# Kernel optimization log

Hardware: AMD Instinct MI355X
Metric: run time of the kernel (lower is better)

## Reference

```python
import jax, jax.numpy as jnp
import numpy as np

B, S, DIM = 2, 2048, 1024
N_HEAD, HEAD_DIM = 16, 64


def setup_inputs() -> dict:
    key = jax.random.key(0)
    k1, k2, k3, k4 = jax.random.split(key, 4)
    x = jax.random.normal(k1, (B, S, DIM), dtype=jnp.float32)
    # rotary table: cos/sin pairs, shape [S, head_dim//2, 2]
    half = HEAD_DIM // 2
    inv_freq = 1.0 / (10000.0 ** (jnp.arange(0, half, dtype=jnp.float32) / half))
    t = jnp.arange(S, dtype=jnp.float32)
    ang = t[:, None] * inv_freq[None, :]
    freqs_cis = jnp.stack([jnp.cos(ang), jnp.sin(ang)], axis=-1)  # [S, half, 2]
    # causal boolean mask [1,1,S,S] (True = attend)
    mask = jnp.tril(jnp.ones((S, S), dtype=bool))[None, None]
    wqkv = jax.random.normal(k2, (3 * DIM, DIM), dtype=jnp.float32) * (DIM ** -0.5)
    wo = jax.random.normal(k3, (DIM, DIM), dtype=jnp.float32) * (DIM ** -0.5)
    return {"x": x, "freqs_cis": freqs_cis, "mask": mask, "wqkv": wqkv, "wo": wo}


def apply_rotary_emb(x, freqs_cis):
    # x: [B, S, H, D]; freqs_cis: [S, D//2, 2]
    xs = x.reshape(*x.shape[:-1], -1, 2)  # [B,S,H,D//2,2]
    fc = freqs_cis[None, :, None, :, :]  # [1,S,1,D//2,2]
    xr, xi = xs[..., 0], xs[..., 1]
    cr, ci = fc[..., 0], fc[..., 1]
    out = jnp.stack([xr * cr - xi * ci, xi * cr + xr * ci], axis=-1)
    return out.reshape(x.shape)


def reference(x, freqs_cis, mask, wqkv, wo):
    bsz, seqlen, _ = x.shape
    qkv = jnp.einsum('bsd,ed->bse', x, wqkv)  # [B,S,3*dim]
    q, k, v = jnp.split(qkv, 3, axis=-1)
    q = q.reshape(bsz, seqlen, N_HEAD, HEAD_DIM)
    k = k.reshape(bsz, seqlen, N_HEAD, HEAD_DIM)
    v = v.reshape(bsz, seqlen, N_HEAD, HEAD_DIM)
    q = apply_rotary_emb(q, freqs_cis)
    k = apply_rotary_emb(k, freqs_cis)
    scale = HEAD_DIM ** -0.5
    scores = jnp.einsum('bqhd,bkhd->bhqk', q, k) * scale  # [B,H,S,S]
    scores = jnp.where(mask, scores, jnp.finfo(scores.dtype).min)
    attn = jax.nn.softmax(scores, axis=-1)
    y = jnp.einsum('bhqk,bkhd->bqhd', attn, v).reshape(bsz, seqlen, N_HEAD * HEAD_DIM)
    return jnp.einsum('bse,de->bsd', y, wo)
```

## Files before the change

### kernel.cpp

```cpp
#include <hip/hip_runtime.h>
#include <hip/hip_bf16.h>
#include <stdint.h>


typedef __attribute__((ext_vector_type(8))) __bf16 bf16x8;
typedef __attribute__((ext_vector_type(4))) float f32x4;
typedef __attribute__((ext_vector_type(16))) float f32x16;

union B8 { uint4 u; bf16x8 v; unsigned short us[8]; };

static __device__ __forceinline__ float bf2f(unsigned short u) {
  union { unsigned int ui; float f; } x; x.ui = ((unsigned int)u) << 16; return x.f;
}
static __device__ __forceinline__ unsigned short f2bf(float f) {
  union { float f; unsigned int ui; } x; x.f = f;
  unsigned int r = x.ui + 0x7fffu + ((x.ui >> 16) & 1u);
  return (unsigned short)(r >> 16);
}
static __device__ __forceinline__ unsigned int cvt_pk_bf16(float lo, float hi) {
  unsigned int r;
  asm("v_cvt_pk_bf16_f32 %0, %1, %2" : "=v"(r) : "v"(lo), "v"(hi));
  return r;
}
static __device__ __forceinline__ f32x4 mfma16(bf16x8 a, bf16x8 b, f32x4 c) {
  return __builtin_amdgcn_mfma_f32_16x16x32_bf16(a, b, c, 0, 0, 0);
}
static __device__ __forceinline__ f32x16 mfma32(bf16x8 a, bf16x8 b, f32x16 c) {
  return __builtin_amdgcn_mfma_f32_32x32x16_bf16(a, b, c, 0, 0, 0);
}
#define AS1 __attribute__((address_space(1)))
#define AS3 __attribute__((address_space(3)))
static __device__ __forceinline__ void gload_lds16(const void* g, void* l) {
  __builtin_amdgcn_global_load_lds((const AS1 unsigned int*)g,
                                   (AS3 unsigned int*)l, 16, 0, 0);
}

__global__ __launch_bounds__(256) void cvt_all_kernel(
    const float* __restrict__ x, const float* __restrict__ wqkv,
    const float* __restrict__ wo,
    unsigned short* __restrict__ xb, unsigned short* __restrict__ wqkvb,
    unsigned short* __restrict__ wob) {
  int i = blockIdx.x * 256 + threadIdx.x;
  const float* src; unsigned short* dst; int off;
  if (i < 1048576)       { src = x;    dst = xb;    off = i; }
  else if (i < 1835008)  { src = wqkv; dst = wqkvb; off = i - 1048576; }
  else                   { src = wo;   dst = wob;   off = i - 1835008; }
  float4 f = ((const float4*)src)[off];
  ushort4 u;
  u.x = f2bf(f.x); u.y = f2bf(f.y); u.z = f2bf(f.z); u.w = f2bf(f.w);
  ((ushort4*)dst)[off] = u;
}

__global__ __launch_bounds__(256) void qkv_rope_kernel(
    const unsigned short* __restrict__ xb,
    const unsigned short* __restrict__ wqkvb,
    const float* __restrict__ freqs,
    unsigned short* __restrict__ Q,
    unsigned short* __restrict__ K,
    unsigned short* __restrict__ Vt)
{
  __shared__ __align__(16) unsigned short As[128 * 64];
  __shared__ __align__(16) unsigned short Bs[128 * 64];
  const int t = threadIdx.x;
  const int lane = t & 63, wv = t >> 6;
  const int l31 = lane & 31, lh = lane >> 5;
  const int wm = wv >> 1, wn = wv & 1;
  const int tm = blockIdx.x & 31, tn = blockIdx.x >> 5;
  const int m0 = tm * 128, n0 = tn * 128;

  f32x16 acc[2][2] = {};

  for (int k0 = 0; k0 < 1024; k0 += 64) {
    for (int r = 0; r < 4; ++r) {
      int cid = t + 256 * r;
      int row = cid >> 3, jc = cid & 7;
      int sc = jc ^ (row & 7);
      gload_lds16(xb    + (size_t)(m0 + row) * 1024 + k0 + sc * 8, (char*)As + cid * 16);
      gload_lds16(wqkvb + (size_t)(n0 + row) * 1024 + k0 + sc * 8, (char*)Bs + cid * 16);
    }
    __syncthreads();
    for (int kst = 0; kst < 4; ++kst) {
      const int g = kst * 2 + lh;
      bf16x8 a[2], b[2];
      for (int s2 = 0; s2 < 2; ++s2) {
        int ra = wm * 64 + s2 * 32 + l31;
        a[s2] = *(const bf16x8*)((const char*)As + ra * 128 + (g ^ (ra & 7)) * 16);
        int rb = wn * 64 + s2 * 32 + l31;
        b[s2] = *(const bf16x8*)((const char*)Bs + rb * 128 + (g ^ (rb & 7)) * 16);
      }
      for (int sm = 0; sm < 2; ++sm)
        for (int sn = 0; sn < 2; ++sn)
          acc[sm][sn] = mfma32(a[sm], b[sn], acc[sm][sn]);
    }
    __syncthreads();
  }

  for (int sm = 0; sm < 2; ++sm) {
    for (int sn = 0; sn < 2; ++sn) {
      const int e = n0 + wn * 64 + sn * 32 + l31;
      const int seg = e >> 10;
      const int eh = e & 1023;
      const int h = eh >> 6, d = eh & 63;
      for (int r = 0; r < 16; ++r) {
        const int m = m0 + wm * 64 + sm * 32 + (r & 3) + 8 * (r >> 2) + 4 * lh;
        const int b_ = m >> 11, s_ = m & 2047;
        float v = acc[sm][sn][r];
        if (seg == 2) {
          Vt[((size_t)(b_ * 16 + h) * 64 + d) * 2048 + s_] = f2bf(v);
        } else {
          float partner = __shfl_xor(v, 1, 64);
          float2 fc = *(const float2*)(freqs + s_ * 64 + (d & ~1));
          float outv = (d & 1) ? (v * fc.x + partner * fc.y)
                               : (v * fc.x - partner * fc.y);
          unsigned short* dst = (seg == 0) ? Q : K;
          dst[((size_t)(b_ * 16 + h) * 2048 + s_) * 64 + d] = f2bf(outv);
        }
      }
    }
  }
}

struct QState {
  bf16x8 qf0, qf1;
  f32x4 o[4];
  float lp;
};

static __device__ __forceinline__ void load_q(QState& st,
    const unsigned short* Qb, int q0, int c, int quad) {
  st.qf0 = *(const bf16x8*)(Qb + (q0 + c) * 64 + quad * 8);
  st.qf1 = *(const bf16x8*)(Qb + (q0 + c) * 64 + 32 + quad * 8);
}

static __device__ __forceinline__ void attn_chunk(
    QState& st, const char* Ks, const char* Vs, unsigned short* myp,
    int c, int quad, int k0, int q0, bool diag)
{
  f32x4 sfr[4];
  for (int kc = 0; kc < 4; ++kc) {
    const int key = kc * 16 + c;
    const int s0 = quad ^ (key & 7), s1 = (4 + quad) ^ (key & 7);
    f32x4 sacc = {};
    sacc = mfma16(*(const bf16x8*)(Ks + key * 128 + s0 * 16), st.qf0, sacc);
    sacc = mfma16(*(const bf16x8*)(Ks + key * 128 + s1 * 16), st.qf1, sacc);
    sfr[kc] = sacc;
  }
  const int qrow = q0 + c;
  float e[4][4];
  float lsum = 0.f;
  for (int kc = 0; kc < 4; ++kc) {
    for (int i = 0; i < 4; ++i) {
      float arg = fmaf(sfr[kc][i], 0.18033688f, -20.19773057f);
      if (diag && (k0 + kc * 16 + quad * 4 + i > qrow)) arg = -1e30f;
      e[kc][i] = exp2f(arg);
    }
    lsum += (e[kc][0] + e[kc][1]) + (e[kc][2] + e[kc][3]);
  }
  st.lp += lsum;
  for (int kc = 0; kc < 4; ++kc) {
    uint2 w;
    w.x = cvt_pk_bf16(e[kc][0], e[kc][1]);
    w.y = cvt_pk_bf16(e[kc][2], e[kc][3]);
    *(uint2*)(myp + c * 72 + kc * 16 + quad * 4) = w;
  }
  bf16x8 pf[2];
  pf[0] = *(const bf16x8*)(myp + c * 72 + quad * 8);
  pf[1] = *(const bf16x8*)(myp + c * 72 + 32 + quad * 8);
  for (int ct = 0; ct < 4; ++ct) {
    const int d = ct * 16 + c;
    const int s0 = quad ^ (d & 7), s1 = (4 + quad) ^ (d & 7);
    st.o[ct] = mfma16(pf[0], *(const bf16x8*)(Vs + d * 128 + s0 * 16), st.o[ct]);
    st.o[ct] = mfma16(pf[1], *(const bf16x8*)(Vs + d * 128 + s1 * 16), st.o[ct]);
  }
}

__global__ __launch_bounds__(256) void attn_partial_kernel(
    const unsigned short* __restrict__ Q,
    const unsigned short* __restrict__ K,
    const unsigned short* __restrict__ Vt,
    unsigned short* __restrict__ Po,
    float* __restrict__ Pl)
{
  __shared__ __align__(16) unsigned short Ks[64 * 64];
  __shared__ __align__(16) unsigned short Vs[64 * 64];
  __shared__ __align__(16) unsigned short plds[4][16 * 72];
  const int t = threadIdx.x;
  const int lane = t & 63, wv = t >> 6;
  const int c = lane & 15, quad = lane >> 4;
  const int bh = blockIdx.x & 31;
  const int rest = blockIdx.x >> 5;
  const int j = rest >> 1, half = rest & 1;
  const int qA = j * 64 + wv * 16;
  const int qB = (31 - j) * 64 + wv * 16;

  const unsigned short* Qb = Q + (size_t)bh * (2048 * 64);
  const unsigned short* Kb = K + (size_t)bh * (2048 * 64);
  const unsigned short* Vb = Vt + (size_t)bh * (64 * 2048);

  QState A = {}, Bst = {};
  load_q(A, Qb, qA, c, quad);
  load_q(Bst, Qb, qB, c, quad);

  unsigned short* myp = plds[wv];
  const int ktmax = 31 - j;

  for (int kt = half; kt <= ktmax; kt += 2) {
    const int k0 = kt * 64;
    __syncthreads();
    for (int r = 0; r < 2; ++r) {
      int cid = t + 256 * r;
      int row = cid >> 3, jc = cid & 7;
      int sc = jc ^ (row & 7);
      gload_lds16(Kb + (size_t)(k0 + row) * 64 + sc * 8, (char*)Ks + cid * 16);
      gload_lds16(Vb + (size_t)row * 2048 + k0 + sc * 8, (char*)Vs + cid * 16);
    }
    __syncthreads();
    attn_chunk(Bst, (const char*)Ks, (const char*)Vs, myp, c, quad,
               k0, qB, kt == ktmax);
    if (kt <= j)
      attn_chunk(A, (const char*)Ks, (const char*)Vs, myp, c, quad,
                 k0, qA, kt == j);
  }

  unsigned short* Poh = Po + (size_t)half * (32 * 2048 * 64) + (size_t)bh * (2048 * 64);
  float* Plh = Pl + (size_t)half * (32 * 2048) + bh * 2048;
  for (int set = 0; set < 2; ++set) {
    QState& st = set ? Bst : A;
    const int q0 = set ? qB : qA;
    float l = st.lp;
    l += __shfl_xor(l, 16, 64);
    l += __shfl_xor(l, 32, 64);
    for (int i = 0; i < 4; ++i) {
      const int s = q0 + quad * 4 + i;
      for (int ct = 0; ct < 4; ++ct)
        Poh[(size_t)s * 64 + ct * 16 + c] = f2bf(st.o[ct][i]);
    }
    if (quad == 0) Plh[q0 + c] = l;
  }
}

__global__ __launch_bounds__(256) void combine_kernel(
    const unsigned short* __restrict__ Po, const float* __restrict__ Pl,
    unsigned short* __restrict__ Yb)
{
  const int idx = blockIdx.x * 256 + threadIdx.x;
  const int bh = idx >> 14, rem = idx & 16383;
  const int s = rem >> 3, g = rem & 7;
  const size_t base = (size_t)bh * (2048 * 64) + (size_t)s * 64 + g * 8;
  B8 a, b;
  a.u = *(const uint4*)(Po + base);
  b.u = *(const uint4*)(Po + (size_t)(32 * 2048 * 64) + base);
  float l = Pl[bh * 2048 + s] + Pl[32 * 2048 + bh * 2048 + s];
  float inv = 1.0f / l;
  B8 y;
  for (int k = 0; k < 8; ++k)
    y.us[k] = f2bf((bf2f(a.us[k]) + bf2f(b.us[k])) * inv);
  const int b_ = bh >> 4, h = bh & 15;
  *(uint4*)(Yb + ((size_t)(b_ * 2048 + s)) * 1024 + h * 64 + g * 8) = y.u;
}

__global__ __launch_bounds__(256) void attn_kernel(
    const unsigned short* __restrict__ Q,
    const unsigned short* __restrict__ K,
    const unsigned short* __restrict__ Vt,
    unsigned short* __restrict__ Y)
{
  __shared__ __align__(16) unsigned short Ks[64 * 64];
  __shared__ __align__(16) unsigned short Vs[64 * 64];
  __shared__ __align__(16) unsigned short plds[4][16 * 72];
  const int t = threadIdx.x;
  const int lane = t & 63, wv = t >> 6;
  const int c = lane & 15, quad = lane >> 4;
  const int j = blockIdx.x >> 5, bh = blockIdx.x & 31;
  const int b = bh >> 4, h = bh & 15;
  const int qA = j * 64 + wv * 16;
  const int qB = (31 - j) * 64 + wv * 16;

  const unsigned short* Qb = Q + (size_t)bh * (2048 * 64);
  const unsigned short* Kb = K + (size_t)bh * (2048 * 64);
  const unsigned short* Vb = Vt + (size_t)bh * (64 * 2048);

  QState A = {}, Bst = {};
  load_q(A, Qb, qA, c, quad);
  load_q(Bst, Qb, qB, c, quad);

  const int nkt = 32 - j;
  unsigned short* myp = plds[wv];

  for (int kt = 0; kt < nkt; ++kt) {
    const int k0 = kt * 64;
    __syncthreads();
    for (int r = 0; r < 2; ++r) {
      int cid = t + 256 * r;
      int row = cid >> 3, jc = cid & 7;
      int sc = jc ^ (row & 7);
      gload_lds16(Kb + (size_t)(k0 + row) * 64 + sc * 8, (char*)Ks + cid * 16);
      gload_lds16(Vb + (size_t)row * 2048 + k0 + sc * 8, (char*)Vs + cid * 16);
    }
    __syncthreads();
    attn_chunk(Bst, (const char*)Ks, (const char*)Vs, myp, c, quad,
               k0, qB, kt == 31 - j);
    if (kt <= j)
      attn_chunk(A, (const char*)Ks, (const char*)Vs, myp, c, quad,
                 k0, qA, kt == j);
  }

  for (int set = 0; set < 2; ++set) {
    QState& st = set ? Bst : A;
    const int q0 = set ? qB : qA;
    float l = st.lp;
    l += __shfl_xor(l, 16, 64);
    l += __shfl_xor(l, 32, 64);
    for (int i = 0; i < 4; ++i) {
      float inv = 1.0f / __shfl(l, quad * 4 + i, 64);
      const int s = q0 + quad * 4 + i;
      unsigned short* dst = Y + ((size_t)(b * 2048 + s)) * 1024 + h * 64;
      for (int ct = 0; ct < 4; ++ct)
        dst[ct * 16 + c] = f2bf(st.o[ct][i] * inv);
    }
  }
}

__global__ __launch_bounds__(256) void out_proj_kernel(
    const unsigned short* __restrict__ Y,
    const unsigned short* __restrict__ wob,
    float* __restrict__ out)
{
  __shared__ __align__(16) unsigned short As[128 * 64];
  __shared__ __align__(16) unsigned short Bs[64 * 64];
  const int t = threadIdx.x;
  const int lane = t & 63, wv = t >> 6;
  const int l31 = lane & 31, lh = lane >> 5;
  const int wm = wv >> 1, wn = wv & 1;
  const int blk = blockIdx.x;
  const int tm = (blk & 7) * 4 + ((blk >> 3) & 3);
  const int tn = blk >> 5;
  const int m0 = tm * 128, n0 = tn * 64;

  f32x16 acc[2] = {};

  for (int k0 = 0; k0 < 1024; k0 += 64) {
    for (int r = 0; r < 4; ++r) {
      int cid = t + 256 * r;
      int row = cid >> 3, jc = cid & 7;
      int sc = jc ^ (row & 7);
      gload_lds16(Y + (size_t)(m0 + row) * 1024 + k0 + sc * 8, (char*)As + cid * 16);
    }
    for (int r = 0; r < 2; ++r) {
      int cid = t + 256 * r;
      int row = cid >> 3, jc = cid & 7;
      int sc = jc ^ (row & 7);
      gload_lds16(wob + (size_t)(n0 + row) * 1024 + k0 + sc * 8, (char*)Bs + cid * 16);
    }
    __syncthreads();
    for (int kst = 0; kst < 4; ++kst) {
      const int g = kst * 2 + lh;
      bf16x8 a[2], b;
      for (int s2 = 0; s2 < 2; ++s2) {
        int ra = wm * 64 + s2 * 32 + l31;
        a[s2] = *(const bf16x8*)((const char*)As + ra * 128 + (g ^ (ra & 7)) * 16);
      }
      int rb = wn * 32 + l31;
      b = *(const bf16x8*)((const char*)Bs + rb * 128 + (g ^ (rb & 7)) * 16);
      acc[0] = mfma32(a[0], b, acc[0]);
      acc[1] = mfma32(a[1], b, acc[1]);
    }
    __syncthreads();
  }

  const int col = n0 + wn * 32 + l31;
  for (int sm = 0; sm < 2; ++sm)
    for (int r = 0; r < 16; ++r) {
      const int m = m0 + wm * 64 + sm * 32 + (r & 3) + 8 * (r >> 2) + 4 * lh;
      out[(size_t)m * 1024 + col] = acc[sm][r];
    }
}

extern "C" void kernel_launch(void* const* d_in, const int* in_sizes, int n_in,
                              void* d_out, int out_size, void* d_ws, size_t ws_size,
                              hipStream_t stream) {
  const float* x     = (const float*)d_in[0];
  const float* freqs = (const float*)d_in[1];
  const float* wqkv  = (const float*)d_in[3];
  const float* wo    = (const float*)d_in[4];
  float* out = (float*)d_out;

  const size_t BHSD = (size_t)2 * 16 * 2048 * 64;
  unsigned short* Q     = (unsigned short*)d_ws;
  unsigned short* K     = Q + BHSD;
  unsigned short* Vt    = K + BHSD;
  unsigned short* Yb    = Vt + BHSD;
  unsigned short* xb    = Yb + BHSD;
  unsigned short* wqkvb = xb + 4194304;
  unsigned short* wob   = wqkvb + 3145728;
  unsigned short* Po    = wob + 1048576;
  float*          Pl    = (float*)(Po + 2 * BHSD);

  const size_t need_fast =
      (size_t)((char*)(Pl + 2 * 32 * 2048) - (char*)d_ws);

  cvt_all_kernel<<<8192, 256, 0, stream>>>(x, wqkv, wo, xb, wqkvb, wob);
  qkv_rope_kernel<<<768, 256, 0, stream>>>(xb, wqkvb, freqs, Q, K, Vt);
  if (ws_size >= need_fast) {
    attn_partial_kernel<<<1024, 256, 0, stream>>>(Q, K, Vt, Po, Pl);
    combine_kernel<<<2048, 256, 0, stream>>>(Po, Pl, Yb);
  } else {
    attn_kernel<<<512, 256, 0, stream>>>(Q, K, Vt, Yb);
  }
  out_proj_kernel<<<512, 256, 0, stream>>>(Yb, wob, out);
}
```

Baseline: 215.1 us.

## Double-buffer LDS in QKV and out-proj GEMMs, enlarge QKV tiles

```diff
diff --git a/kernel.cpp b/kernel.cpp
--- a/kernel.cpp
+++ b/kernel.cpp
@@ -51,7 +51,7 @@
   ((ushort4*)dst)[off] = u;
 }
 
-__global__ __launch_bounds__(256) void qkv_rope_kernel(
+__global__ __launch_bounds__(512) void qkv_rope_kernel(
     const unsigned short* __restrict__ xb,
     const unsigned short* __restrict__ wqkvb,
     const float* __restrict__ freqs,
@@ -59,45 +59,66 @@
     unsigned short* __restrict__ K,
     unsigned short* __restrict__ Vt)
 {
-  __shared__ __align__(16) unsigned short As[128 * 64];
-  __shared__ __align__(16) unsigned short Bs[128 * 64];
+  __shared__ __align__(16) unsigned short As[2][256 * 64];
+  __shared__ __align__(16) unsigned short Bs[2][192 * 64];
   const int t = threadIdx.x;
   const int lane = t & 63, wv = t >> 6;
   const int l31 = lane & 31, lh = lane >> 5;
   const int wm = wv >> 1, wn = wv & 1;
-  const int tm = blockIdx.x & 31, tn = blockIdx.x >> 5;
-  const int m0 = tm * 128, n0 = tn * 128;
-
-  f32x16 acc[2][2] = {};
-
-  for (int k0 = 0; k0 < 1024; k0 += 64) {
-    for (int r = 0; r < 4; ++r) {
-      int cid = t + 256 * r;
-      int row = cid >> 3, jc = cid & 7;
-      int sc = jc ^ (row & 7);
-      gload_lds16(xb    + (size_t)(m0 + row) * 1024 + k0 + sc * 8, (char*)As + cid * 16);
-      gload_lds16(wqkvb + (size_t)(n0 + row) * 1024 + k0 + sc * 8, (char*)Bs + cid * 16);
-    }
-    __syncthreads();
+  const int blk = blockIdx.x;
+  const int xcd = blk & 7, j = blk >> 3;
+  const int tm = 2 * xcd + (j >> 4), tn = j & 15;
+  const int m0 = tm * 256, n0 = tn * 192;
+
+  f32x16 acc[2][3] = {};
+
+  auto stage = [&](int bb, int k0) {
+    for (int r = 0; r < 7; ++r) {
+      int cid = t + 512 * r;
+      if (cid < 2048) {
+        int row = cid >> 3, jc = cid & 7, sc = jc ^ (row & 7);
+        gload_lds16(xb + (size_t)(m0 + row) * 1024 + k0 + sc * 8,
+                    (char*)As[bb] + cid * 16);
+      } else {
+        int c2 = cid - 2048;
+        int row = c2 >> 3, jc = c2 & 7, sc = jc ^ (row & 7);
+        gload_lds16(wqkvb + (size_t)(n0 + row) * 1024 + k0 + sc * 8,
+                    (char*)Bs[bb] + c2 * 16);
+      }
+    }
+  };
+
+  auto compute = [&](const char* Ap, const char* Bp) {
     for (int kst = 0; kst < 4; ++kst) {
       const int g = kst * 2 + lh;
-      bf16x8 a[2], b[2];
-      for (int s2 = 0; s2 < 2; ++s2) {
-        int ra = wm * 64 + s2 * 32 + l31;
-        a[s2] = *(const bf16x8*)((const char*)As + ra * 128 + (g ^ (ra & 7)) * 16);
-        int rb = wn * 64 + s2 * 32 + l31;
-        b[s2] = *(const bf16x8*)((const char*)Bs + rb * 128 + (g ^ (rb & 7)) * 16);
+      bf16x8 a[2], b[3];
+      for (int sm = 0; sm < 2; ++sm) {
+        int ra = wm * 64 + sm * 32 + l31;
+        a[sm] = *(const bf16x8*)(Ap + ra * 128 + (g ^ (ra & 7)) * 16);
+      }
+      for (int sn = 0; sn < 3; ++sn) {
+        int rb = wn * 96 + sn * 32 + l31;
+        b[sn] = *(const bf16x8*)(Bp + rb * 128 + (g ^ (rb & 7)) * 16);
       }
       for (int sm = 0; sm < 2; ++sm)
-        for (int sn = 0; sn < 2; ++sn)
+        for (int sn = 0; sn < 3; ++sn)
           acc[sm][sn] = mfma32(a[sm], b[sn], acc[sm][sn]);
     }
-    __syncthreads();
+  };
+
+  stage(0, 0);
+  for (int t2 = 0; t2 < 16; t2 += 2) {
+    __syncthreads();
+    stage(1, (t2 + 1) * 64);
+    compute((const char*)As[0], (const char*)Bs[0]);
+    __syncthreads();
+    if (t2 < 14) stage(0, (t2 + 2) * 64);
+    compute((const char*)As[1], (const char*)Bs[1]);
   }
 
   for (int sm = 0; sm < 2; ++sm) {
-    for (int sn = 0; sn < 2; ++sn) {
-      const int e = n0 + wn * 64 + sn * 32 + l31;
+    for (int sn = 0; sn < 3; ++sn) {
+      const int e = n0 + wn * 96 + sn * 32 + l31;
       const int seg = e >> 10;
       const int eh = e & 1023;
       const int h = eh >> 6, d = eh & 63;
@@ -326,8 +347,8 @@
     const unsigned short* __restrict__ wob,
     float* __restrict__ out)
 {
-  __shared__ __align__(16) unsigned short As[128 * 64];
-  __shared__ __align__(16) unsigned short Bs[64 * 64];
+  __shared__ __align__(16) unsigned short As[2][128 * 64];
+  __shared__ __align__(16) unsigned short Bs[2][64 * 64];
   const int t = threadIdx.x;
   const int lane = t & 63, wv = t >> 6;
   const int l31 = lane & 31, lh = lane >> 5;
@@ -339,33 +360,45 @@
 
   f32x16 acc[2] = {};
 
-  for (int k0 = 0; k0 < 1024; k0 += 64) {
-    for (int r = 0; r < 4; ++r) {
+  auto stage = [&](int bb, int k0) {
+    for (int r = 0; r < 6; ++r) {
       int cid = t + 256 * r;
-      int row = cid >> 3, jc = cid & 7;
-      int sc = jc ^ (row & 7);
-      gload_lds16(Y + (size_t)(m0 + row) * 1024 + k0 + sc * 8, (char*)As + cid * 16);
-    }
-    for (int r = 0; r < 2; ++r) {
-      int cid = t + 256 * r;
-      int row = cid >> 3, jc = cid & 7;
-      int sc = jc ^ (row & 7);
-      gload_lds16(wob + (size_t)(n0 + row) * 1024 + k0 + sc * 8, (char*)Bs + cid * 16);
-    }
-    __syncthreads();
+      if (cid < 1024) {
+        int row = cid >> 3, jc = cid & 7, sc = jc ^ (row & 7);
+        gload_lds16(Y + (size_t)(m0 + row) * 1024 + k0 + sc * 8,
+                    (char*)As[bb] + cid * 16);
+      } else {
+        int c2 = cid - 1024;
+        int row = c2 >> 3, jc = c2 & 7, sc = jc ^ (row & 7);
+        gload_lds16(wob + (size_t)(n0 + row) * 1024 + k0 + sc * 8,
+                    (char*)Bs[bb] + c2 * 16);
+      }
+    }
+  };
+
+  auto compute = [&](const char* Ap, const char* Bp) {
     for (int kst = 0; kst < 4; ++kst) {
       const int g = kst * 2 + lh;
       bf16x8 a[2], b;
-      for (int s2 = 0; s2 < 2; ++s2) {
-        int ra = wm * 64 + s2 * 32 + l31;
-        a[s2] = *(const bf16x8*)((const char*)As + ra * 128 + (g ^ (ra & 7)) * 16);
+      for (int sm = 0; sm < 2; ++sm) {
+        int ra = wm * 64 + sm * 32 + l31;
+        a[sm] = *(const bf16x8*)(Ap + ra * 128 + (g ^ (ra & 7)) * 16);
       }
       int rb = wn * 32 + l31;
-      b = *(const bf16x8*)((const char*)Bs + rb * 128 + (g ^ (rb & 7)) * 16);
+      b = *(const bf16x8*)(Bp + rb * 128 + (g ^ (rb & 7)) * 16);
       acc[0] = mfma32(a[0], b, acc[0]);
       acc[1] = mfma32(a[1], b, acc[1]);
     }
-    __syncthreads();
+  };
+
+  stage(0, 0);
+  for (int t2 = 0; t2 < 16; t2 += 2) {
+    __syncthreads();
+    stage(1, (t2 + 1) * 64);
+    compute((const char*)As[0], (const char*)Bs[0]);
+    __syncthreads();
+    if (t2 < 14) stage(0, (t2 + 2) * 64);
+    compute((const char*)As[1], (const char*)Bs[1]);
   }
 
   const int col = n0 + wn * 32 + l31;
@@ -400,7 +433,7 @@
       (size_t)((char*)(Pl + 2 * 32 * 2048) - (char*)d_ws);
 
   cvt_all_kernel<<<8192, 256, 0, stream>>>(x, wqkv, wo, xb, wqkvb, wob);
-  qkv_rope_kernel<<<768, 256, 0, stream>>>(xb, wqkvb, freqs, Q, K, Vt);
+  qkv_rope_kernel<<<256, 512, 0, stream>>>(xb, wqkvb, freqs, Q, K, Vt);
   if (ws_size >= need_fast) {
     attn_partial_kernel<<<1024, 256, 0, stream>>>(Q, K, Vt, Po, Pl);
     combine_kernel<<<2048, 256, 0, stream>>>(Po, Pl, Yb);
```

Result: no change. 214.2 us (-0.4%).
